# Optimization experiments

Measured on AMD Instinct MI355X. Metric: run time of the kernel, lower is better.

The kernel has to match this reference:

```python
import jax, jax.numpy as jnp
import numpy as np

EPS = 1e-12
N_HEADS = 16


def _ln(x, g, b, eps=EPS):
    m = jnp.mean(x, axis=-1, keepdims=True)
    v = jnp.var(x, axis=-1, keepdims=True)
    return (x - m) * jax.lax.rsqrt(v + eps) * g + b


def setup_inputs() -> dict:
    key = jax.random.key(0)
    ks = jax.random.split(key, 8)
    B, S, D, I = 2, 2048, 1024, 4096
    s = 0.02
    f32 = jnp.float32
    return {
        "x": jax.random.normal(ks[0], (B, S, D), f32),
        "input_mask": jnp.zeros((B, 1, 1, S), f32),  # additive mask, 0 = no masking
        "norm_w": jnp.ones((D,), f32),
        "norm_b": jnp.zeros((D,), f32),
        "attn_qkvw": jax.random.normal(ks[1], (D, 3 * D), f32) * s,
        "attn_qkvb": jnp.zeros((3 * D,), f32),
        "attn_ow": jax.random.normal(ks[2], (D, D), f32) * s,
        "attn_ob": jnp.zeros((D,), f32),
        "attn_nw": jnp.ones((D,), f32),
        "attn_nb": jnp.zeros((D,), f32),
        "inter_w": jax.random.normal(ks[3], (D, I), f32) * s,
        "inter_b": jnp.zeros((I,), f32),
        "inter_w1": jax.random.normal(ks[4], (D, I), f32) * s,
        "output_w": jax.random.normal(ks[5], (I, D), f32) * s,
        "output_b": jnp.zeros((D,), f32),
    }


def reference(x, input_mask, norm_w, norm_b, attn_qkvw, attn_qkvb, attn_ow,
              attn_ob, attn_nw, attn_nb, inter_w, inter_b, inter_w1,
              output_w, output_b):
    B, S, D = x.shape
    hd = D // N_HEADS

    # --- fused qkv_gemm: pre-layernorm + QKV GEMM + bias ---
    ln1 = _ln(x, norm_w, norm_b)
    qkv = ln1 @ attn_qkvw + attn_qkvb            # [B,S,3D]
    q, k, v = jnp.split(qkv, 3, axis=-1)

    def to_heads(t):  # [B,S,D] -> [B,H,S,hd]
        return t.reshape(B, S, N_HEADS, hd).transpose(0, 2, 1, 3)

    q, k, v = to_heads(q), to_heads(k), to_heads(v)

    # --- softmax-context attention (scale_attention=True -> 1/sqrt(head_dim)) ---
    scores = jnp.einsum('bhqd,bhkd->bhqk', q, k) / jnp.sqrt(jnp.float32(hd))
    scores = scores + input_mask                 # additive mask [B,1,1,S]
    probs = jax.nn.softmax(scores, axis=-1)
    ctx = jnp.einsum('bhqk,bhkd->bhqd', probs, v)
    ctx = ctx.transpose(0, 2, 1, 3).reshape(B, S, D)

    attn_out = ctx @ attn_ow                     # vector_matmul (no bias)

    # --- fused mlp_gemm: bias+residual add, layernorm, GEMM+bias+gelu ---
    residual_add = attn_out + attn_ob + x
    ln2 = _ln(residual_add, attn_nw, attn_nb)
    intermediate = jax.nn.gelu(ln2 @ inter_w + inter_b, approximate=False)
    # gated path: vector_matmul(mlp input, inter_w1) * intermediate (per source)
    intermediate = (attn_out @ inter_w1) * intermediate

    # --- output projection + bias_residual ---
    out = intermediate @ output_w + output_b + residual_add
    return out
```

## Files before the change

### kernel.cpp

```cpp
#include <hip/hip_runtime.h>
#include <hip/hip_bf16.h>

#define BATCH 2
#define SEQ   2048
#define DIM   1024
#define IDIM  4096
#define NH    16
#define HD    64
#define TOK   (BATCH * SEQ)

typedef __hip_bfloat16 bf16;

typedef short bf16x8_t __attribute__((ext_vector_type(8)));
typedef float f32x4_t  __attribute__((ext_vector_type(4)));

__device__ __forceinline__ float ldv(const float* p, size_t i) { return p[i]; }
__device__ __forceinline__ float ldv(const bf16*  p, size_t i) { return __bfloat162float(p[i]); }
__device__ __forceinline__ void  stv(float* p, size_t i, float v) { p[i] = v; }
__device__ __forceinline__ void  stv(bf16*  p, size_t i, float v) { p[i] = __float2bfloat16(v); }

__device__ __forceinline__ f32x4_t mfma16(bf16x8_t a, bf16x8_t b, f32x4_t c) {
    return __builtin_amdgcn_mfma_f32_16x16x32_bf16(a, b, c, 0, 0, 0);
}

__device__ __forceinline__ void gload16(const bf16* g, bf16* l) {
    __builtin_amdgcn_global_load_lds(
        (const __attribute__((address_space(1))) void*)g,
        (__attribute__((address_space(3))) void*)l, 16, 0, 0);
}

__global__ __launch_bounds__(256) void ln_kernel(const float* __restrict__ in,
                                                 const float* __restrict__ w,
                                                 const float* __restrict__ b,
                                                 bf16* __restrict__ out) {
    const int row = blockIdx.x;
    const int tid = threadIdx.x;
    const float* xr = in + (size_t)row * DIM;

    float v[4], sum = 0.f, sq = 0.f;
#pragma unroll
    for (int i = 0; i < 4; i++) {
        float t = xr[tid + i * 256];
        v[i] = t; sum += t; sq += t * t;
    }
#pragma unroll
    for (int off = 32; off >= 1; off >>= 1) {
        sum += __shfl_xor(sum, off);
        sq  += __shfl_xor(sq,  off);
    }
    __shared__ float s1[4], s2[4];
    int wid = tid >> 6;
    if ((tid & 63) == 0) { s1[wid] = sum; s2[wid] = sq; }
    __syncthreads();
    sum = s1[0] + s1[1] + s1[2] + s1[3];
    sq  = s2[0] + s2[1] + s2[2] + s2[3];

    const float mean = sum * (1.f / DIM);
    const float var  = fmaxf(sq * (1.f / DIM) - mean * mean, 0.f);
    const float rstd = rsqrtf(var + 1e-12f);

    bf16* orow = out + (size_t)row * DIM;
#pragma unroll
    for (int i = 0; i < 4; i++) {
        int idx = tid + i * 256;
        orow[idx] = __float2bfloat16((v[i] - mean) * rstd * w[idx] + b[idx]);
    }
}

__global__ __launch_bounds__(256) void wconv_kernel(const float* __restrict__ W,
                                                    bf16* __restrict__ Wt,
                                                    int K, int N) {
    __shared__ float tile[32][33];
    const int tid = threadIdx.x;
    const int n0 = blockIdx.x * 32;
    const int k0 = blockIdx.y * 32;
    const int c = tid & 31;
    const int r = tid >> 5;
#pragma unroll
    for (int i = 0; i < 4; i++)
        tile[r + i * 8][c] = W[(size_t)(k0 + r + i * 8) * N + n0 + c];
    __syncthreads();
#pragma unroll
    for (int i = 0; i < 4; i++)
        Wt[(size_t)(n0 + r + i * 8) * K + k0 + c] = __float2bfloat16(tile[c][r + i * 8]);
}

#define GBK 32

template<typename TX, int MODE, int TM, int TN>
__global__ __launch_bounds__(256) void mgemm_kernel(const bf16* __restrict__ A,
                                                    const bf16* __restrict__ Bt,
                                                    const float* __restrict__ bias,
                                                    const TX* __restrict__ aux,
                                                    TX* __restrict__ C,
                                                    const float* __restrict__ bias2,
                                                    const float* __restrict__ xin,
                                                    float* __restrict__ C2,
                                                    int M, int N, int K) {
    constexpr int TILE_M = TM * 32;
    constexpr int TILE_N = TN * 32;
    __shared__ alignas(16) bf16 As[TILE_M][GBK];
    __shared__ alignas(16) bf16 Bs[TILE_N][GBK];

    const int tid  = threadIdx.x;
    const int w    = tid >> 6;
    const int lane = tid & 63;
    const int cl   = lane & 15;
    const int qd   = lane >> 4;
    const int wm   = w >> 1;
    const int wn   = w & 1;

    const int gn   = gridDim.x;
    const int lin  = blockIdx.y * gn + blockIdx.x;
    const int span = 8 * gn;
    const int panel = lin / span;
    const int rem   = lin - panel * span;
    const int by    = panel * 8 + (rem & 7);
    const int bx    = rem >> 3;

    const int row0 = by * TILE_M;
    const int col0 = bx * TILE_N;

    const int lrow = lane >> 2;
    const int lkg  = lane & 3;

    f32x4_t acc[TM][TN];
#pragma unroll
    for (int m = 0; m < TM; m++)
#pragma unroll
        for (int n = 0; n < TN; n++) acc[m][n] = {0.f, 0.f, 0.f, 0.f};

    for (int k0 = 0; k0 < K; k0 += GBK) {
        __syncthreads();
#pragma unroll
        for (int i = 0; i < TM / 2; i++) {
            const int r16 = (w * (TM / 2) + i) * 16;
            gload16(A + (size_t)(row0 + r16 + lrow) * K + k0 + lkg * 8, &As[r16][0]);
        }
#pragma unroll
        for (int j = 0; j < TN / 2; j++) {
            const int r16 = (w * (TN / 2) + j) * 16;
            gload16(Bt + (size_t)(col0 + r16 + lrow) * K + k0 + lkg * 8, &Bs[r16][0]);
        }
        __syncthreads();

        bf16x8_t af[TM], bfr[TN];
#pragma unroll
        for (int m = 0; m < TM; m++)
            af[m] = *(const bf16x8_t*)&As[wm * (TM * 16) + m * 16 + cl][qd * 8];
#pragma unroll
        for (int n = 0; n < TN; n++)
            bfr[n] = *(const bf16x8_t*)&Bs[wn * (TN * 16) + n * 16 + cl][qd * 8];
#pragma unroll
        for (int m = 0; m < TM; m++)
#pragma unroll
            for (int n = 0; n < TN; n++)
                acc[m][n] = mfma16(af[m], bfr[n], acc[m][n]);
    }

#pragma unroll
    for (int m = 0; m < TM; m++) {
#pragma unroll
        for (int n = 0; n < TN; n++) {
            const int gc = col0 + wn * (TN * 16) + n * 16 + cl;
            const float bv = (MODE != 2 && MODE != 4 && bias) ? bias[gc] : 0.f;
#pragma unroll
            for (int r = 0; r < 4; r++) {
                const int gr = row0 + wm * (TM * 16) + m * 16 + qd * 4 + r;
                float c = acc[m][n][r] + bv;
                if (MODE == 1) {
                    c = 0.5f * c * (1.f + erff(c * 0.70710678118654752f));
                } else if (MODE == 2) {
                    c *= ldv(aux, (size_t)gr * N + gc);
                } else if (MODE == 3) {
                    c += ldv(aux, (size_t)gr * N + gc);
                }
                stv(C, (size_t)gr * N + gc, c);
                if (MODE == 4) {
                    C2[(size_t)gr * N + gc] = c + bias2[gc] + xin[(size_t)gr * N + gc];
                }
            }
        }
    }
}

__global__ __launch_bounds__(256) void vtrans_kernel(const bf16* __restrict__ qkv,
                                                     bf16* __restrict__ vt) {
    __shared__ bf16 t[64][72];
    const int tid = threadIdx.x;
    const int s0  = blockIdx.x * 64;
    const int bh  = blockIdx.y;
    const int bb  = bh >> 4;
    const int h   = bh & 15;
    const bf16* src = qkv + (size_t)bb * SEQ * (3 * DIM) + 2 * DIM + h * HD;
    const int r  = tid >> 3;
    const int cc = tid & 7;
#pragma unroll
    for (int i = 0; i < 2; i++)
        *(bf16x8_t*)&t[r + i * 32][cc * 8] =
            *(const bf16x8_t*)(src + (size_t)(s0 + r + i * 32) * (3 * DIM) + cc * 8);
    __syncthreads();
    bf16* dst = vt + (size_t)bh * HD * SEQ + s0;
#pragma unroll
    for (int i = 0; i < 2; i++) {
        const int d = r + i * 32;
        bf16x8_t v;
#pragma unroll
        for (int j = 0; j < 8; j++)
            ((short*)&v)[j] = *(const short*)&t[cc * 8 + j][d];
        *(bf16x8_t*)(dst + (size_t)d * SEQ + cc * 8) = v;
    }
}

#define KCH 64
#define NCH (SEQ / KCH)

__device__ __forceinline__ unsigned pk2(float lo, float hi) {
    unsigned a = (unsigned)__bfloat16_as_ushort(__float2bfloat16(lo));
    unsigned b = (unsigned)__bfloat16_as_ushort(__float2bfloat16(hi));
    return a | (b << 16);
}

union PAU { bf16x8_t v; unsigned u[4]; };

__global__ __launch_bounds__(256, 2) void attn_mfma_kernel(const bf16* __restrict__ qkv,
                                                           const bf16* __restrict__ vt,
                                                           const float* __restrict__ mask,
                                                           bf16* __restrict__ ctx) {
    __shared__ alignas(16) bf16 Kl[2][KCH][64];
    __shared__ alignas(16) bf16 Vl[2][KCH][64];

    const int tid  = threadIdx.x;
    const int w    = tid >> 6;
    const int lane = tid & 63;
    const int cl   = lane & 15;
    const int qd   = lane >> 4;
    const int c7   = cl & 7;

    const int qtile = blockIdx.x;
    const int bh    = blockIdx.y;
    const int bb    = bh >> 4;
    const int h     = bh & 15;

    const bf16*  base = qkv + (size_t)bb * SEQ * (3 * DIM) + h * HD;
    const bf16*  gK   = base + DIM;
    const bf16*  gV   = vt + (size_t)bh * HD * SEQ;
    const float* mrow = mask + (size_t)bb * SEQ;

    bf16x8_t aq[2][2];
#pragma unroll
    for (int qt = 0; qt < 2; qt++) {
        const bf16* qrow = base + (size_t)(qtile * 128 + w * 32 + qt * 16 + cl) * (3 * DIM);
        aq[qt][0] = *(const bf16x8_t*)(qrow + qd * 8);
        aq[qt][1] = *(const bf16x8_t*)(qrow + 32 + qd * 8);
    }

    const bf16x8_t onesv = {0x3F80, 0x3F80, 0x3F80, 0x3F80,
                            0x3F80, 0x3F80, 0x3F80, 0x3F80};

    const int sr  = lane >> 3;
    const int scw = (lane & 7) ^ sr;

#pragma unroll
    for (int i = 0; i < 2; i++) {
        const int row = i * 32 + w * 8 + sr;
        gload16(gK + (size_t)row * (3 * DIM) + scw * 8, &Kl[0][i * 32 + w * 8][0]);
        gload16(gV + (size_t)row * SEQ + scw * 8, &Vl[0][i * 32 + w * 8][0]);
    }
    f32x4_t mkx[4];
#pragma unroll
    for (int ks = 0; ks < 4; ks++)
        mkx[ks] = *(const f32x4_t*)&mrow[ks * 16 + qd * 4];

    f32x4_t O[2][4];
#pragma unroll
    for (int qt = 0; qt < 2; qt++)
#pragma unroll
        for (int ns = 0; ns < 4; ns++) O[qt][ns] = {0.f, 0.f, 0.f, 0.f};
    f32x4_t li[2] = {{0.f,0.f,0.f,0.f},{0.f,0.f,0.f,0.f}};

    for (int c = 0; c < NCH; c++) {
        __syncthreads();
        const bf16 (*Kb)[64] = Kl[c & 1];
        const bf16 (*Vb)[64] = Vl[c & 1];

        f32x4_t mk[4];
#pragma unroll
        for (int ks = 0; ks < 4; ks++) mk[ks] = mkx[ks];

        if (c + 1 < NCH) {
            bf16 (*Kn)[64] = Kl[(c + 1) & 1];
            bf16 (*Vn)[64] = Vl[(c + 1) & 1];
            const int k0n = (c + 1) * KCH;
#pragma unroll
            for (int i = 0; i < 2; i++) {
                const int row = i * 32 + w * 8 + sr;
                gload16(gK + (size_t)(k0n + row) * (3 * DIM) + scw * 8, &Kn[i * 32 + w * 8][0]);
                gload16(gV + (size_t)row * SEQ + k0n + scw * 8, &Vn[i * 32 + w * 8][0]);
            }
#pragma unroll
            for (int ks = 0; ks < 4; ks++)
                mkx[ks] = *(const f32x4_t*)&mrow[k0n + ks * 16 + qd * 4];
        }

        bf16x8_t kf[4][2];
#pragma unroll
        for (int ks = 0; ks < 4; ks++) {
            kf[ks][0] = *(const bf16x8_t*)&Kb[ks * 16 + cl][(qd ^ c7) << 3];
            kf[ks][1] = *(const bf16x8_t*)&Kb[ks * 16 + cl][((4 + qd) ^ c7) << 3];
        }

        PAU pa[2][2];
#pragma unroll
        for (int qt = 0; qt < 2; qt++) {
            unsigned Dv[4][2];
#pragma unroll
            for (int ks = 0; ks < 4; ks++) {
                f32x4_t s = {0.f, 0.f, 0.f, 0.f};
                s = mfma16(kf[ks][0], aq[qt][0], s);
                s = mfma16(kf[ks][1], aq[qt][1], s);
                const float e0 = __expf(s[0] * 0.125f + mk[ks][0]);
                const float e1 = __expf(s[1] * 0.125f + mk[ks][1]);
                const float e2 = __expf(s[2] * 0.125f + mk[ks][2]);
                const float e3 = __expf(s[3] * 0.125f + mk[ks][3]);
                Dv[ks][0] = pk2(e0, e1);
                Dv[ks][1] = pk2(e2, e3);
            }
#pragma unroll
            for (int rp = 0; rp < 2; rp++) {
                auto z0 = __builtin_amdgcn_permlane32_swap(Dv[0][rp], Dv[1][rp], false, false);
                auto w0 = __builtin_amdgcn_permlane16_swap(z0[0], z0[1], false, false);
                pa[qt][0].u[rp]     = w0[0];
                pa[qt][0].u[rp + 2] = w0[1];
                auto z1 = __builtin_amdgcn_permlane32_swap(Dv[2][rp], Dv[3][rp], false, false);
                auto w1 = __builtin_amdgcn_permlane16_swap(z1[0], z1[1], false, false);
                pa[qt][1].u[rp]     = w1[0];
                pa[qt][1].u[rp + 2] = w1[1];
            }
            f32x4_t ls = {0.f, 0.f, 0.f, 0.f};
            ls = mfma16(pa[qt][0].v, onesv, ls);
            ls = mfma16(pa[qt][1].v, onesv, ls);
            li[qt] += ls;
        }

#pragma unroll
        for (int ns = 0; ns < 4; ns++) {
            bf16x8_t v0 = *(const bf16x8_t*)&Vb[ns * 16 + cl][(qd ^ c7) << 3];
            bf16x8_t v1 = *(const bf16x8_t*)&Vb[ns * 16 + cl][((4 + qd) ^ c7) << 3];
#pragma unroll
            for (int qt = 0; qt < 2; qt++) {
                O[qt][ns] = mfma16(pa[qt][0].v, v0, O[qt][ns]);
                O[qt][ns] = mfma16(pa[qt][1].v, v1, O[qt][ns]);
            }
        }
    }

#pragma unroll
    for (int qt = 0; qt < 2; qt++) {
#pragma unroll
        for (int r = 0; r < 4; r++) {
            const int row = qtile * 128 + w * 32 + qt * 16 + qd * 4 + r;
            bf16* orow = ctx + (size_t)(bb * SEQ + row) * DIM + h * HD;
            const float inv = 1.f / li[qt][r];
#pragma unroll
            for (int ns = 0; ns < 4; ns++)
                orow[ns * 16 + cl] = __float2bfloat16(O[qt][ns][r] * inv);
        }
    }
}

extern "C" void kernel_launch(void* const* d_in, const int* in_sizes, int n_in,
                              void* d_out, int out_size, void* d_ws, size_t ws_size,
                              hipStream_t stream) {
    const float* x        = (const float*)d_in[0];
    const float* mask     = (const float*)d_in[1];
    const float* norm_w   = (const float*)d_in[2];
    const float* norm_b   = (const float*)d_in[3];
    const float* qkvw     = (const float*)d_in[4];
    const float* qkvb     = (const float*)d_in[5];
    const float* attn_ow  = (const float*)d_in[6];
    const float* attn_ob  = (const float*)d_in[7];
    const float* attn_nw  = (const float*)d_in[8];
    const float* attn_nb  = (const float*)d_in[9];
    const float* inter_w  = (const float*)d_in[10];
    const float* inter_b  = (const float*)d_in[11];
    const float* inter_w1 = (const float*)d_in[12];
    const float* output_w = (const float*)d_in[13];
    const float* output_b = (const float*)d_in[14];

    float* out = (float*)d_out;
    bf16*  ws  = (bf16*)d_ws;

    const size_t M1 = 1024 * 1024;
    bf16* ln_s      = ws;
    bf16* qkv       = ws + 4 * M1;
    bf16* inter     = ws + 4 * M1;
    bf16* qkvw_t    = ws + 16 * M1;
    bf16* attn_owt  = ws + 19 * M1;
    bf16* vt        = ws + 20 * M1;
    bf16* attn_out  = ws + 20 * M1;
    bf16* inter_wt  = ws + 24 * M1;
    bf16* inter_w1t = ws + 28 * M1;
    bf16* output_wt = ws + 32 * M1;
    float* resid    = out;

    dim3 blk(256);

    wconv_kernel<<<dim3(3072 / 32, 1024 / 32), blk, 0, stream>>>(qkvw,     qkvw_t,    1024, 3072);
    wconv_kernel<<<dim3(1024 / 32, 1024 / 32), blk, 0, stream>>>(attn_ow,  attn_owt,  1024, 1024);
    wconv_kernel<<<dim3(4096 / 32, 1024 / 32), blk, 0, stream>>>(inter_w,  inter_wt,  1024, 4096);
    wconv_kernel<<<dim3(4096 / 32, 1024 / 32), blk, 0, stream>>>(inter_w1, inter_w1t, 1024, 4096);
    wconv_kernel<<<dim3(1024 / 32, 4096 / 32), blk, 0, stream>>>(output_w, output_wt, 4096, 1024);

    ln_kernel<<<TOK, blk, 0, stream>>>(x, norm_w, norm_b, ln_s);

    mgemm_kernel<bf16, 0, 4, 4><<<dim3(3072 / 128, TOK / 128), blk, 0, stream>>>(
        ln_s, qkvw_t, qkvb, (const bf16*)nullptr, qkv,
        nullptr, nullptr, nullptr, TOK, 3 * DIM, DIM);

    vtrans_kernel<<<dim3(SEQ / 64, BATCH * NH), blk, 0, stream>>>(qkv, vt);

    attn_mfma_kernel<<<dim3(SEQ / 128, BATCH * NH), blk, 0, stream>>>(qkv, vt, mask, ln_s);

    mgemm_kernel<bf16, 4, 4, 2><<<dim3(DIM / 64, TOK / 128), blk, 0, stream>>>(
        ln_s, attn_owt, (const float*)nullptr, (const bf16*)nullptr, attn_out,
        attn_ob, x, resid, TOK, DIM, DIM);

    ln_kernel<<<TOK, blk, 0, stream>>>(resid, attn_nw, attn_nb, ln_s);

    mgemm_kernel<bf16, 1, 4, 4><<<dim3(IDIM / 128, TOK / 128), blk, 0, stream>>>(
        ln_s, inter_wt, inter_b, (const bf16*)nullptr, inter,
        nullptr, nullptr, nullptr, TOK, IDIM, DIM);

    mgemm_kernel<bf16, 2, 4, 4><<<dim3(IDIM / 128, TOK / 128), blk, 0, stream>>>(
        attn_out, inter_w1t, (const float*)nullptr, inter, inter,
        nullptr, nullptr, nullptr, TOK, IDIM, DIM);

    mgemm_kernel<float, 3, 4, 2><<<dim3(DIM / 64, TOK / 128), blk, 0, stream>>>(
        inter, output_wt, output_b, resid, out,
        nullptr, nullptr, nullptr, TOK, DIM, IDIM);
}
```

Baseline: 499.6 us.

## Double-buffer GEMM LDS with swizzle and fuse gated MLP GEMMs into one kernel

The GEMM kernel now double-buffers its LDS tiles, loading the next K slice while computing the current one, and drops to one barrier per iteration. It also applies an XOR swizzle to the 16-byte slots to reduce LDS bank conflicts. The two intermediate GEMMs (GELU branch and gate branch) are merged into a single dual-GEMM kernel that applies GELU and the gating multiply in registers, which removes one write and one read of the large intermediate tensor. The cost is twice the LDS and accumulator registers in the dual kernel, which may lower occupancy.

```diff
diff --git a/kernel.cpp b/kernel.cpp
--- a/kernel.cpp
+++ b/kernel.cpp
@@ -99,8 +99,8 @@
                                                     int M, int N, int K) {
     constexpr int TILE_M = TM * 32;
     constexpr int TILE_N = TN * 32;
-    __shared__ alignas(16) bf16 As[TILE_M][GBK];
-    __shared__ alignas(16) bf16 Bs[TILE_N][GBK];
+    __shared__ alignas(16) bf16 As[2][TILE_M][GBK];
+    __shared__ alignas(16) bf16 Bs[2][TILE_N][GBK];
 
     const int tid  = threadIdx.x;
     const int w    = tid >> 6;
@@ -123,6 +123,11 @@
 
     const int lrow = lane >> 2;
     const int lkg  = lane & 3;
+    const int sslot = lkg ^ ((lrow >> 1) & 3);
+    const int rds   = (cl >> 1) & 3;
+
+    const bf16* gA = A  + (size_t)(row0 + lrow) * K + sslot * 8;
+    const bf16* gB = Bt + (size_t)(col0 + lrow) * K + sslot * 8;
 
     f32x4_t acc[TM][TN];
 #pragma unroll
@@ -130,32 +135,41 @@
 #pragma unroll
         for (int n = 0; n < TN; n++) acc[m][n] = {0.f, 0.f, 0.f, 0.f};
 
-    for (int k0 = 0; k0 < K; k0 += GBK) {
-        __syncthreads();
+    auto stage = [&](int b, int k0) {
 #pragma unroll
         for (int i = 0; i < TM / 2; i++) {
             const int r16 = (w * (TM / 2) + i) * 16;
-            gload16(A + (size_t)(row0 + r16 + lrow) * K + k0 + lkg * 8, &As[r16][0]);
+            gload16(gA + (size_t)r16 * K + k0, &As[b][r16][0]);
         }
 #pragma unroll
         for (int j = 0; j < TN / 2; j++) {
             const int r16 = (w * (TN / 2) + j) * 16;
-            gload16(Bt + (size_t)(col0 + r16 + lrow) * K + k0 + lkg * 8, &Bs[r16][0]);
-        }
-        __syncthreads();
+            gload16(gB + (size_t)r16 * K + k0, &Bs[b][r16][0]);
+        }
+    };
+
+    stage(0, 0);
+    __syncthreads();
+
+    const int NT = K / GBK;
+    for (int t = 0; t < NT; t++) {
+        const int b = t & 1;
+        if (t + 1 < NT) stage(b ^ 1, (t + 1) * GBK);
 
         bf16x8_t af[TM], bfr[TN];
 #pragma unroll
         for (int m = 0; m < TM; m++)
-            af[m] = *(const bf16x8_t*)&As[wm * (TM * 16) + m * 16 + cl][qd * 8];
+            af[m] = *(const bf16x8_t*)&As[b][wm * (TM * 16) + m * 16 + cl][(qd ^ rds) * 8];
 #pragma unroll
         for (int n = 0; n < TN; n++)
-            bfr[n] = *(const bf16x8_t*)&Bs[wn * (TN * 16) + n * 16 + cl][qd * 8];
+            bfr[n] = *(const bf16x8_t*)&Bs[b][wn * (TN * 16) + n * 16 + cl][(qd ^ rds) * 8];
 #pragma unroll
         for (int m = 0; m < TM; m++)
 #pragma unroll
             for (int n = 0; n < TN; n++)
                 acc[m][n] = mfma16(af[m], bfr[n], acc[m][n]);
+
+        __syncthreads();
     }
 
 #pragma unroll
@@ -163,22 +177,133 @@
 #pragma unroll
         for (int n = 0; n < TN; n++) {
             const int gc = col0 + wn * (TN * 16) + n * 16 + cl;
-            const float bv = (MODE != 2 && MODE != 4 && bias) ? bias[gc] : 0.f;
+            const float bv = (MODE != 4 && bias) ? bias[gc] : 0.f;
 #pragma unroll
             for (int r = 0; r < 4; r++) {
                 const int gr = row0 + wm * (TM * 16) + m * 16 + qd * 4 + r;
                 float c = acc[m][n][r] + bv;
-                if (MODE == 1) {
-                    c = 0.5f * c * (1.f + erff(c * 0.70710678118654752f));
-                } else if (MODE == 2) {
-                    c *= ldv(aux, (size_t)gr * N + gc);
-                } else if (MODE == 3) {
+                if (MODE == 3) {
                     c += ldv(aux, (size_t)gr * N + gc);
                 }
                 stv(C, (size_t)gr * N + gc, c);
                 if (MODE == 4) {
                     C2[(size_t)gr * N + gc] = c + bias2[gc] + xin[(size_t)gr * N + gc];
                 }
+            }
+        }
+    }
+}
+
+template<int TM, int TN>
+__global__ __launch_bounds__(256) void dualgemm_kernel(const bf16* __restrict__ A0,
+                                                       const bf16* __restrict__ B0t,
+                                                       const bf16* __restrict__ A1,
+                                                       const bf16* __restrict__ B1t,
+                                                       const float* __restrict__ bias,
+                                                       bf16* __restrict__ C,
+                                                       int M, int N, int K) {
+    constexpr int TILE_M = TM * 32;
+    constexpr int TILE_N = TN * 32;
+    __shared__ alignas(16) bf16 As0[2][TILE_M][GBK];
+    __shared__ alignas(16) bf16 Bs0[2][TILE_N][GBK];
+    __shared__ alignas(16) bf16 As1[2][TILE_M][GBK];
+    __shared__ alignas(16) bf16 Bs1[2][TILE_N][GBK];
+
+    const int tid  = threadIdx.x;
+    const int w    = tid >> 6;
+    const int lane = tid & 63;
+    const int cl   = lane & 15;
+    const int qd   = lane >> 4;
+    const int wm   = w >> 1;
+    const int wn   = w & 1;
+
+    const int gn   = gridDim.x;
+    const int lin  = blockIdx.y * gn + blockIdx.x;
+    const int span = 8 * gn;
+    const int panel = lin / span;
+    const int rem   = lin - panel * span;
+    const int by    = panel * 8 + (rem & 7);
+    const int bx    = rem >> 3;
+
+    const int row0 = by * TILE_M;
+    const int col0 = bx * TILE_N;
+
+    const int lrow = lane >> 2;
+    const int lkg  = lane & 3;
+    const int sslot = lkg ^ ((lrow >> 1) & 3);
+    const int rds   = (cl >> 1) & 3;
+
+    const bf16* gA0 = A0  + (size_t)(row0 + lrow) * K + sslot * 8;
+    const bf16* gB0 = B0t + (size_t)(col0 + lrow) * K + sslot * 8;
+    const bf16* gA1 = A1  + (size_t)(row0 + lrow) * K + sslot * 8;
+    const bf16* gB1 = B1t + (size_t)(col0 + lrow) * K + sslot * 8;
+
+    f32x4_t acc0[TM][TN], acc1[TM][TN];
+#pragma unroll
+    for (int m = 0; m < TM; m++)
+#pragma unroll
+        for (int n = 0; n < TN; n++) {
+            acc0[m][n] = {0.f, 0.f, 0.f, 0.f};
+            acc1[m][n] = {0.f, 0.f, 0.f, 0.f};
+        }
+
+    auto stage = [&](int b, int k0) {
+#pragma unroll
+        for (int i = 0; i < TM / 2; i++) {
+            const int r16 = (w * (TM / 2) + i) * 16;
+            gload16(gA0 + (size_t)r16 * K + k0, &As0[b][r16][0]);
+            gload16(gA1 + (size_t)r16 * K + k0, &As1[b][r16][0]);
+        }
+#pragma unroll
+        for (int j = 0; j < TN / 2; j++) {
+            const int r16 = (w * (TN / 2) + j) * 16;
+            gload16(gB0 + (size_t)r16 * K + k0, &Bs0[b][r16][0]);
+            gload16(gB1 + (size_t)r16 * K + k0, &Bs1[b][r16][0]);
+        }
+    };
+
+    stage(0, 0);
+    __syncthreads();
+
+    const int NT = K / GBK;
+    for (int t = 0; t < NT; t++) {
+        const int b = t & 1;
+        if (t + 1 < NT) stage(b ^ 1, (t + 1) * GBK);
+
+        bf16x8_t af0[TM], af1[TM];
+#pragma unroll
+        for (int m = 0; m < TM; m++) {
+            const int rr = wm * (TM * 16) + m * 16 + cl;
+            af0[m] = *(const bf16x8_t*)&As0[b][rr][(qd ^ rds) * 8];
+            af1[m] = *(const bf16x8_t*)&As1[b][rr][(qd ^ rds) * 8];
+        }
+#pragma unroll
+        for (int n = 0; n < TN; n++) {
+            const int rr = wn * (TN * 16) + n * 16 + cl;
+            bf16x8_t b0 = *(const bf16x8_t*)&Bs0[b][rr][(qd ^ rds) * 8];
+            bf16x8_t b1 = *(const bf16x8_t*)&Bs1[b][rr][(qd ^ rds) * 8];
+#pragma unroll
+            for (int m = 0; m < TM; m++) {
+                acc0[m][n] = mfma16(af0[m], b0, acc0[m][n]);
+                acc1[m][n] = mfma16(af1[m], b1, acc1[m][n]);
+            }
+        }
+
+        __syncthreads();
+    }
+
+#pragma unroll
+    for (int m = 0; m < TM; m++) {
+#pragma unroll
+        for (int n = 0; n < TN; n++) {
+            const int gc = col0 + wn * (TN * 16) + n * 16 + cl;
+            const float bv = bias[gc];
+#pragma unroll
+            for (int r = 0; r < 4; r++) {
+                const int gr = row0 + wm * (TM * 16) + m * 16 + qd * 4 + r;
+                float g = acc0[m][n][r] + bv;
+                g = 0.5f * g * (1.f + erff(g * 0.70710678118654752f));
+                C[(size_t)gr * N + gc] = __float2bfloat16(g * acc1[m][n][r]);
             }
         }
     }
@@ -428,13 +553,8 @@
 
     ln_kernel<<<TOK, blk, 0, stream>>>(resid, attn_nw, attn_nb, ln_s);
 
-    mgemm_kernel<bf16, 1, 4, 4><<<dim3(IDIM / 128, TOK / 128), blk, 0, stream>>>(
-        ln_s, inter_wt, inter_b, (const bf16*)nullptr, inter,
-        nullptr, nullptr, nullptr, TOK, IDIM, DIM);
-
-    mgemm_kernel<bf16, 2, 4, 4><<<dim3(IDIM / 128, TOK / 128), blk, 0, stream>>>(
-        attn_out, inter_w1t, (const float*)nullptr, inter, inter,
-        nullptr, nullptr, nullptr, TOK, IDIM, DIM);
+    dualgemm_kernel<4, 4><<<dim3(IDIM / 128, TOK / 128), blk, 0, stream>>>(
+        ln_s, inter_wt, attn_out, inter_w1t, inter_b, inter, TOK, IDIM, DIM);
 
     mgemm_kernel<float, 3, 4, 2><<<dim3(DIM / 64, TOK / 128), blk, 0, stream>>>(
         inter, output_wt, output_b, resid, out,
```

Result: no change. 504.8 us (+1.0%).
